# Performance work log

Hardware: AMD Instinct MI355X
Metric: run time of the kernel (lower is better)

The kernel has to match this reference:

```python
import jax, jax.numpy as jnp
import numpy as np

NUM_GRAPHS = 8
EV_A3_TO_GPA = 160.21766208


def _energy(pos, bond_vec, src, dst, edge_graph, centers, W1, b1, W2, b2, W3, b3):
    # Surrogate GNN energy: edge displacement mixes pos and bond_vec so both get grads,
    # mirroring grad(total_energies, [pos, bond_vec]) in the original wrapper.
    disp = bond_vec + pos[dst] - pos[src]                      # [E,3]
    d = jnp.sqrt(jnp.sum(disp * disp, axis=-1) + 1e-12)        # [E]
    rbf = jnp.exp(-jnp.square(d[:, None] - centers[None, :]))  # [E,K]
    h = jax.nn.silu(rbf @ W1 + b1)                             # [E,H]
    h = jax.nn.silu(h @ W2 + b2)                               # [E,H]
    e_edge = (h @ W3 + b3)[:, 0]                               # [E]
    return jax.ops.segment_sum(e_edge, edge_graph, num_segments=NUM_GRAPHS)  # [B]


def setup_inputs() -> dict:
    key = jax.random.key(0)
    ks = jax.random.split(key, 8)
    N, E, K, H = 49152, 786432, 32, 64
    pos = jax.random.normal(ks[0], (N, 3), jnp.float32) * 3.0
    bond_vec = jax.random.normal(ks[1], (E, 3), jnp.float32)
    src = jax.random.randint(ks[2], (E,), 0, N, dtype=jnp.int32)
    dst = jax.random.randint(ks[3], (E,), 0, N, dtype=jnp.int32)
    edge_graph = jnp.repeat(jnp.arange(NUM_GRAPHS, dtype=jnp.int32), E // NUM_GRAPHS)
    volume = jax.random.uniform(ks[4], (N,), jnp.float32, 50.0, 150.0)
    centers = jnp.linspace(0.0, 5.0, K).astype(jnp.float32)
    W1 = jax.random.normal(ks[5], (K, H), jnp.float32) / np.float32(np.sqrt(K))
    b1 = jnp.zeros((H,), jnp.float32)
    W2 = jax.random.normal(ks[6], (H, H), jnp.float32) / np.float32(np.sqrt(H))
    b2 = jnp.zeros((H,), jnp.float32)
    W3 = jax.random.normal(ks[7], (H, 1), jnp.float32) / np.float32(np.sqrt(H))
    b3 = jnp.zeros((1,), jnp.float32)
    return {"pos": pos, "bond_vec": bond_vec, "src": src, "dst": dst,
            "edge_graph": edge_graph, "volume": volume, "centers": centers,
            "W1": W1, "b1": b1, "W2": W2, "b2": b2, "W3": W3, "b3": b3}


def reference(pos, bond_vec, src, dst, edge_graph, volume, centers, W1, b1, W2, b2, W3, b3):
    energies, vjp_fn = jax.vjp(
        lambda p, bv: _energy(p, bv, src, dst, edge_graph, centers, W1, b1, W2, b2, W3, b3),
        pos, bond_vec)
    # grad_outputs = ones_like(total_energies)
    gpos, gbv = vjp_fn(jnp.ones_like(energies))
    forces = -gpos                                             # [N,3]
    f_ij = -gbv                                                # [E,3]
    # Per-graph stress: bond_vec_g^T @ f_ij_g, vectorized as segment-summed outer products.
    outer = bond_vec[:, :, None] * f_ij[:, None, :]            # [E,3,3]
    S = jax.ops.segment_sum(outer, edge_graph, num_segments=NUM_GRAPHS)  # [B,3,3]
    nodes_per_graph = pos.shape[0] // NUM_GRAPHS
    vol0 = volume[jnp.arange(NUM_GRAPHS) * nodes_per_graph]    # volume at first node of each graph
    stresses = (-EV_A3_TO_GPA * S / vol0[:, None, None]).reshape(NUM_GRAPHS * 3, 3)
    hessian = jnp.zeros((1,), jnp.float32)                     # calc_hessian=False
    return energies, forces, stresses, hessian
```

## Files before the change

### kernel.cpp

```cpp
#include <hip/hip_runtime.h>
#include <math.h>

#define K_RBF 32
#define H_DIM 64
#define TBL 4096
#define D_MAX 16.0f
#define N_NODES 49152
#define N_EDGES 786432
#define N_GRAPHS 8
#define NODES_PER_GRAPH 6144
#define EV_A3_TO_GPA 160.21766208f
#define LOG2E 1.44269504088896f

#define OUT_FORCES 8
#define OUT_STRESS 147464
#define OUT_TAIL_N 81

#define CHUNK_NODES  192
#define CHUNK_FLOATS 576
#define N_CHUNKS     256

#define EDGE_BLOCKS   512
#define EDGE_THREADS  512
#define EDGES_PER_THREAD 3
#define EDGES_PER_BLOCK (EDGE_THREADS * EDGES_PER_THREAD)
#define EDGES_PER_GRAPH (N_EDGES / N_GRAPHS)
#define BLK_PER_GRAPH 64

#define SLOT_CAP   40

#define LANES_PER_RUN 16
#define RUNS_PER_PASS 64
#define SCT_PASSES    8

#define OFF_TAB 0u
#define OFF_CNT 32768u
#define OFF_REC (32768u + (unsigned)(N_CHUNKS * EDGE_BLOCKS * 4))
#define WS_NEED ((size_t)OFF_REC + (size_t)N_CHUNKS * EDGE_BLOCKS * SLOT_CAP * 16u)

__device__ __forceinline__ int chunk_of(int node) {
    return (int)((unsigned)((node >> 6) * 683) >> 11);
}

__device__ __forceinline__ float2 mlp_entry(
    int i, int lane, const float* __restrict__ centers,
    const float* __restrict__ W1, const float* __restrict__ b1,
    const float* __restrict__ W2s, const float* __restrict__ b2,
    const float* __restrict__ W3, const float* __restrict__ b3)
{
    float d  = (float)i * (D_MAX / (float)TBL);
    float z1 = b1[lane], u = 0.f;
#pragma unroll
    for (int k = 0; k < K_RBF; ++k) {
        float tc = d - centers[k];
        float e  = exp2f(-tc * tc * LOG2E);
        float w  = W1[k * H_DIM + lane];
        z1 = fmaf(e, w, z1);
        u  = fmaf(-2.f * tc * e, w, u);
    }
    float s1  = 1.f / (1.f + exp2f(-z1 * LOG2E));
    float h1  = z1 * s1;
    float ds1 = s1 * fmaf(z1, 1.f - s1, 1.f);

    float z2 = b2[lane];
#pragma unroll
    for (int h = 0; h < H_DIM; ++h)
        z2 = fmaf(__shfl(h1, h, 64), W2s[h * 65 + lane], z2);

    float s2  = 1.f / (1.f + exp2f(-z2 * LOG2E));
    float w3  = W3[lane];
    float Fp  = z2 * s2 * w3;
    float dz2 = w3 * s2 * fmaf(z2, 1.f - s2, 1.f);

    float dh1 = 0.f;
#pragma unroll
    for (int j = 0; j < H_DIM; ++j)
        dh1 = fmaf(__shfl(dz2, j, 64), W2s[lane * 65 + j], dh1);

    float Gp = dh1 * ds1 * u;
#pragma unroll
    for (int m = 32; m > 0; m >>= 1) {
        Fp += __shfl_xor(Fp, m, 64);
        Gp += __shfl_xor(Gp, m, 64);
    }
    return make_float2(Fp + b3[0], Gp);
}

__global__ __launch_bounds__(256) void build_table(
    const float* __restrict__ centers,
    const float* __restrict__ W1, const float* __restrict__ b1,
    const float* __restrict__ W2, const float* __restrict__ b2,
    const float* __restrict__ W3, const float* __restrict__ b3,
    float2* __restrict__ tab, float* __restrict__ out, int zero_out_tail)
{
    if (blockIdx.x == 0 && zero_out_tail) {
        int t = threadIdx.x;
        if (t < N_GRAPHS) out[t] = 0.f;
        else if (t < OUT_TAIL_N) out[3 * N_NODES + t] = 0.f;
    }

    __shared__ float W2s[H_DIM * 65];
    for (int idx = threadIdx.x; idx < H_DIM * H_DIM; idx += 256)
        W2s[(idx >> 6) * 65 + (idx & 63)] = W2[idx];
    __syncthreads();

    int lane = threadIdx.x & 63;
    int i    = blockIdx.x * 4 + (threadIdx.x >> 6);
    float2 fg = mlp_entry(i, lane, centers, W1, b1, W2s, b2, W3, b3);
    if (lane == 0) tab[i] = fg;
}

__global__ __launch_bounds__(EDGE_THREADS) void edge_compute(
    const float* __restrict__ pos, const float* __restrict__ bond,
    const int* __restrict__ src, const int* __restrict__ dst,
    const float* __restrict__ volume, const float2* __restrict__ tab,
    float4* __restrict__ recs, int* __restrict__ cnttab,
    float* __restrict__ out)
{
    __shared__ int   cnt[N_CHUNKS];
    __shared__ float red[8][10];

    const int t = threadIdx.x;
    const int b = blockIdx.x;
    if (t < N_CHUNKS) cnt[t] = 0;
    __syncthreads();

    const int g = b >> 6;
    const int base_e = b * EDGES_PER_BLOCK;

    float vacc[10];
#pragma unroll
    for (int q = 0; q < 10; ++q) vacc[q] = 0.f;

#pragma unroll
    for (int i = 0; i < EDGES_PER_THREAD; ++i) {
        int e  = base_e + i * EDGE_THREADS + t;
        int si = src[e], di = dst[e];
        float bx = bond[3 * e + 0], by = bond[3 * e + 1], bz = bond[3 * e + 2];
        float dx = bx + pos[3 * di + 0] - pos[3 * si + 0];
        float dy = by + pos[3 * di + 1] - pos[3 * si + 1];
        float dz = bz + pos[3 * di + 2] - pos[3 * si + 2];
        float d  = sqrtf(fmaf(dx, dx, fmaf(dy, dy, fmaf(dz, dz, 1e-12f))));

        float tt  = fminf(d * ((float)TBL / D_MAX), (float)(TBL - 1));
        int   ix  = min((int)tt, TBL - 2);
        float fr  = tt - (float)ix;
        float2 ta = tab[ix], tb2 = tab[ix + 1];
        float F = fmaf(fr, tb2.x - ta.x, ta.x);
        float G = fmaf(fr, tb2.y - ta.y, ta.y);

        float scl = G / d;
        float gx = scl * dx, gy = scl * dy, gz = scl * dz;

        int c0 = chunk_of(di), c1 = chunk_of(si);
        int r0 = atomicAdd(&cnt[c0], 1);
        int r1 = atomicAdd(&cnt[c1], 1);
        if (r0 < SLOT_CAP)
            recs[((size_t)c0 * EDGE_BLOCKS + b) * SLOT_CAP + r0] =
                make_float4(-gx, -gy, -gz, __int_as_float(di - c0 * CHUNK_NODES));
        if (r1 < SLOT_CAP)
            recs[((size_t)c1 * EDGE_BLOCKS + b) * SLOT_CAP + r1] =
                make_float4(gx, gy, gz, __int_as_float(si - c1 * CHUNK_NODES));

        vacc[0] += F;
        vacc[1] = fmaf(bx, gx, vacc[1]); vacc[2] = fmaf(bx, gy, vacc[2]);
        vacc[3] = fmaf(bx, gz, vacc[3]); vacc[4] = fmaf(by, gx, vacc[4]);
        vacc[5] = fmaf(by, gy, vacc[5]); vacc[6] = fmaf(by, gz, vacc[6]);
        vacc[7] = fmaf(bz, gx, vacc[7]); vacc[8] = fmaf(bz, gy, vacc[8]);
        vacc[9] = fmaf(bz, gz, vacc[9]);
    }

#pragma unroll
    for (int q = 0; q < 10; ++q) {
        float x = vacc[q];
#pragma unroll
        for (int m = 32; m > 0; m >>= 1) x += __shfl_xor(x, m, 64);
        vacc[q] = x;
    }
    int wave = t >> 6;
    if ((t & 63) == 0)
#pragma unroll
        for (int q = 0; q < 10; ++q) red[wave][q] = vacc[q];
    __syncthreads();

    if (t < N_CHUNKS)
        cnttab[(size_t)t * EDGE_BLOCKS + b] = min(cnt[t], SLOT_CAP);

    if (t < 10) {
        float tot = 0.f;
#pragma unroll
        for (int k = 0; k < 8; ++k) tot += red[k][t];
        if (t == 0) atomicAdd(out + g, tot);
        else {
            float vol = volume[g * NODES_PER_GRAPH];
            atomicAdd(out + OUT_STRESS + g * 9 + (t - 1),
                      tot * (EV_A3_TO_GPA / vol));
        }
    }
}

__global__ __launch_bounds__(1024) void scatter_direct(
    const float4* __restrict__ recs, const int* __restrict__ cnttab,
    float* __restrict__ out)
{
    __shared__ float acc[CHUNK_FLOATS];
    __shared__ int   cl[EDGE_BLOCKS];
    const int t = threadIdx.x;
    const int c = blockIdx.x;
    if (t < CHUNK_FLOATS) acc[t] = 0.f;
    if (t < EDGE_BLOCKS) cl[t] = cnttab[(size_t)c * EDGE_BLOCKS + t];
    __syncthreads();

    const float4* seg = recs + (size_t)c * EDGE_BLOCKS * SLOT_CAP;
    const int sub = t & (LANES_PER_RUN - 1);
    const int rr0 = t >> 4;
#pragma unroll
    for (int p = 0; p < SCT_PASSES; ++p) {
        int rr  = p * RUNS_PER_PASS + rr0;
        int n   = cl[rr];
        const float4* run = seg + (size_t)rr * SLOT_CAP;
        for (int s = sub; s < n; s += LANES_PER_RUN) {
            float4 rec = run[s];
            int li = 3 * __float_as_int(rec.w);
            atomicAdd(&acc[li + 0], rec.x);
            atomicAdd(&acc[li + 1], rec.y);
            atomicAdd(&acc[li + 2], rec.z);
        }
    }
    __syncthreads();

    if (t < CHUNK_FLOATS)
        out[OUT_FORCES + c * CHUNK_FLOATS + t] = acc[t];
}

__global__ __launch_bounds__(256) void edge_fallback(
    const float* __restrict__ pos, const float* __restrict__ bond,
    const int* __restrict__ src, const int* __restrict__ dst,
    const float* __restrict__ volume, const float2* __restrict__ tab,
    float* __restrict__ out)
{
    __shared__ float red[4][10];
    int lb = (blockIdx.x & 7) * (EDGES_PER_GRAPH / 256) + (blockIdx.x >> 3);
    int g  = blockIdx.x & 7;
    int e  = lb * 256 + threadIdx.x;

    int si = src[e], di = dst[e];
    float bx = bond[3 * e + 0], by = bond[3 * e + 1], bz = bond[3 * e + 2];
    float dx = bx + pos[3 * di + 0] - pos[3 * si + 0];
    float dy = by + pos[3 * di + 1] - pos[3 * si + 1];
    float dz = bz + pos[3 * di + 2] - pos[3 * si + 2];
    float d  = sqrtf(fmaf(dx, dx, fmaf(dy, dy, fmaf(dz, dz, 1e-12f))));

    float tt  = fminf(d * ((float)TBL / D_MAX), (float)(TBL - 1));
    int   ix  = min((int)tt, TBL - 2);
    float fr  = tt - (float)ix;
    float2 ta = tab[ix], tb2 = tab[ix + 1];
    float F = fmaf(fr, tb2.x - ta.x, ta.x);
    float G = fmaf(fr, tb2.y - ta.y, ta.y);
    float scl = G / d;
    float gx = scl * dx, gy = scl * dy, gz = scl * dz;

    float* forces = out + OUT_FORCES;
    atomicAdd(forces + 3 * di + 0, -gx);
    atomicAdd(forces + 3 * di + 1, -gy);
    atomicAdd(forces + 3 * di + 2, -gz);
    atomicAdd(forces + 3 * si + 0,  gx);
    atomicAdd(forces + 3 * si + 1,  gy);
    atomicAdd(forces + 3 * si + 2,  gz);

    float v[10] = { F,
                    bx * gx, bx * gy, bx * gz,
                    by * gx, by * gy, by * gz,
                    bz * gx, bz * gy, bz * gz };
#pragma unroll
    for (int q = 0; q < 10; ++q) {
        float x = v[q];
#pragma unroll
        for (int m = 32; m > 0; m >>= 1) x += __shfl_xor(x, m, 64);
        v[q] = x;
    }
    int wave = threadIdx.x >> 6;
    if ((threadIdx.x & 63) == 0)
#pragma unroll
        for (int q = 0; q < 10; ++q) red[wave][q] = v[q];
    __syncthreads();
    if (threadIdx.x < 10) {
        float tot = red[0][threadIdx.x] + red[1][threadIdx.x]
                  + red[2][threadIdx.x] + red[3][threadIdx.x];
        if (threadIdx.x == 0) atomicAdd(out + g, tot);
        else {
            float vol = volume[g * NODES_PER_GRAPH];
            atomicAdd(out + OUT_STRESS + g * 9 + (threadIdx.x - 1),
                      tot * (EV_A3_TO_GPA / vol));
        }
    }
}

extern "C" void kernel_launch(void* const* d_in, const int* in_sizes, int n_in,
                              void* d_out, int out_size, void* d_ws, size_t ws_size,
                              hipStream_t stream)
{
    const float* pos     = (const float*)d_in[0];
    const float* bond    = (const float*)d_in[1];
    const int*   src     = (const int*)d_in[2];
    const int*   dst     = (const int*)d_in[3];
    const float* volume  = (const float*)d_in[5];
    const float* centers = (const float*)d_in[6];
    const float* W1 = (const float*)d_in[7];
    const float* b1 = (const float*)d_in[8];
    const float* W2 = (const float*)d_in[9];
    const float* b2 = (const float*)d_in[10];
    const float* W3 = (const float*)d_in[11];
    const float* b3 = (const float*)d_in[12];
    float*  out    = (float*)d_out;
    char*   ws     = (char*)d_ws;
    float2* tab    = (float2*)(ws + OFF_TAB);
    int*    cnttab = (int*)(ws + OFF_CNT);
    float4* recs   = (float4*)(ws + OFF_REC);

    if (ws_size >= WS_NEED) {
        build_table<<<TBL / 4, 256, 0, stream>>>(centers, W1, b1, W2, b2, W3, b3,
                                                 tab, out, 1);
        edge_compute<<<EDGE_BLOCKS, EDGE_THREADS, 0, stream>>>(
            pos, bond, src, dst, volume, tab, recs, cnttab, out);
        scatter_direct<<<N_CHUNKS, 1024, 0, stream>>>(recs, cnttab, out);
    } else {
        hipMemsetAsync(d_out, 0, (size_t)out_size * sizeof(float), stream);
        build_table<<<TBL / 4, 256, 0, stream>>>(centers, W1, b1, W2, b2, W3, b3,
                                                 tab, out, 0);
        edge_fallback<<<N_EDGES / 256, 256, 0, stream>>>(
            pos, bond, src, dst, volume, tab, out);
    }
}
```

Before: 154.4 us.

## Replace bucketed record scatter with direct global atomic force accumulation

Removes the two-pass scheme, in which per-chunk force records went to workspace and a separate scatter kernel reduced them in shared memory. Edge threads now atomically add force contributions straight into global memory after a memset, and the edge kernel is relaunched with more, smaller blocks. This saves the record write/read traffic and one kernel launch. In exchange it adds 6 global float atomics per edge with random addresses and a memset of the whole output.

Measured after the change: 346.5 us. 2.24x slower.

```diff
diff --git a/kernel.cpp b/kernel.cpp
--- a/kernel.cpp
+++ b/kernel.cpp
@@ -14,33 +14,16 @@
 
 #define OUT_FORCES 8
 #define OUT_STRESS 147464
-#define OUT_TAIL_N 81
 
-#define CHUNK_NODES  192
-#define CHUNK_FLOATS 576
-#define N_CHUNKS     256
-
-#define EDGE_BLOCKS   512
-#define EDGE_THREADS  512
+#define EDGE_BLOCKS   1024
+#define EDGE_THREADS  256
 #define EDGES_PER_THREAD 3
 #define EDGES_PER_BLOCK (EDGE_THREADS * EDGES_PER_THREAD)
 #define EDGES_PER_GRAPH (N_EDGES / N_GRAPHS)
-#define BLK_PER_GRAPH 64
-
-#define SLOT_CAP   40
-
-#define LANES_PER_RUN 16
-#define RUNS_PER_PASS 64
-#define SCT_PASSES    8
+#define BLK_PER_GRAPH 128
 
 #define OFF_TAB 0u
-#define OFF_CNT 32768u
-#define OFF_REC (32768u + (unsigned)(N_CHUNKS * EDGE_BLOCKS * 4))
-#define WS_NEED ((size_t)OFF_REC + (size_t)N_CHUNKS * EDGE_BLOCKS * SLOT_CAP * 16u)
-
-__device__ __forceinline__ int chunk_of(int node) {
-    return (int)((unsigned)((node >> 6) * 683) >> 11);
-}
+#define WS_NEED 32768u
 
 __device__ __forceinline__ float2 mlp_entry(
     int i, int lane, const float* __restrict__ centers,
@@ -91,14 +74,8 @@
     const float* __restrict__ W1, const float* __restrict__ b1,
     const float* __restrict__ W2, const float* __restrict__ b2,
     const float* __restrict__ W3, const float* __restrict__ b3,
-    float2* __restrict__ tab, float* __restrict__ out, int zero_out_tail)
+    float2* __restrict__ tab)
 {
-    if (blockIdx.x == 0 && zero_out_tail) {
-        int t = threadIdx.x;
-        if (t < N_GRAPHS) out[t] = 0.f;
-        else if (t < OUT_TAIL_N) out[3 * N_NODES + t] = 0.f;
-    }
-
     __shared__ float W2s[H_DIM * 65];
     for (int idx = threadIdx.x; idx < H_DIM * H_DIM; idx += 256)
         W2s[(idx >> 6) * 65 + (idx & 63)] = W2[idx];
@@ -110,23 +87,19 @@
     if (lane == 0) tab[i] = fg;
 }
 
-__global__ __launch_bounds__(EDGE_THREADS) void edge_compute(
+__global__ __launch_bounds__(EDGE_THREADS) void edge_direct(
     const float* __restrict__ pos, const float* __restrict__ bond,
     const int* __restrict__ src, const int* __restrict__ dst,
     const float* __restrict__ volume, const float2* __restrict__ tab,
-    float4* __restrict__ recs, int* __restrict__ cnttab,
     float* __restrict__ out)
 {
-    __shared__ int   cnt[N_CHUNKS];
-    __shared__ float red[8][10];
+    __shared__ float red[4][10];
 
     const int t = threadIdx.x;
     const int b = blockIdx.x;
-    if (t < N_CHUNKS) cnt[t] = 0;
-    __syncthreads();
-
-    const int g = b >> 6;
+    const int g = b >> 7;
     const int base_e = b * EDGES_PER_BLOCK;
+    float* __restrict__ forces = out + OUT_FORCES;
 
     float vacc[10];
 #pragma unroll
@@ -152,15 +125,12 @@
         float scl = G / d;
         float gx = scl * dx, gy = scl * dy, gz = scl * dz;
 
-        int c0 = chunk_of(di), c1 = chunk_of(si);
-        int r0 = atomicAdd(&cnt[c0], 1);
-        int r1 = atomicAdd(&cnt[c1], 1);
-        if (r0 < SLOT_CAP)
-            recs[((size_t)c0 * EDGE_BLOCKS + b) * SLOT_CAP + r0] =
-                make_float4(-gx, -gy, -gz, __int_as_float(di - c0 * CHUNK_NODES));
-        if (r1 < SLOT_CAP)
-            recs[((size_t)c1 * EDGE_BLOCKS + b) * SLOT_CAP + r1] =
-                make_float4(gx, gy, gz, __int_as_float(si - c1 * CHUNK_NODES));
+        atomicAdd(forces + 3 * di + 0, -gx);
+        atomicAdd(forces + 3 * di + 1, -gy);
+        atomicAdd(forces + 3 * di + 2, -gz);
+        atomicAdd(forces + 3 * si + 0,  gx);
+        atomicAdd(forces + 3 * si + 1,  gy);
+        atomicAdd(forces + 3 * si + 2,  gz);
 
         vacc[0] += F;
         vacc[1] = fmaf(bx, gx, vacc[1]); vacc[2] = fmaf(bx, gy, vacc[2]);
@@ -182,115 +152,12 @@
 #pragma unroll
         for (int q = 0; q < 10; ++q) red[wave][q] = vacc[q];
     __syncthreads();
-
-    if (t < N_CHUNKS)
-        cnttab[(size_t)t * EDGE_BLOCKS + b] = min(cnt[t], SLOT_CAP);
-
     if (t < 10) {
-        float tot = 0.f;
-#pragma unroll
-        for (int k = 0; k < 8; ++k) tot += red[k][t];
+        float tot = red[0][t] + red[1][t] + red[2][t] + red[3][t];
         if (t == 0) atomicAdd(out + g, tot);
         else {
             float vol = volume[g * NODES_PER_GRAPH];
             atomicAdd(out + OUT_STRESS + g * 9 + (t - 1),
-                      tot * (EV_A3_TO_GPA / vol));
-        }
-    }
-}
-
-__global__ __launch_bounds__(1024) void scatter_direct(
-    const float4* __restrict__ recs, const int* __restrict__ cnttab,
-    float* __restrict__ out)
-{
-    __shared__ float acc[CHUNK_FLOATS];
-    __shared__ int   cl[EDGE_BLOCKS];
-    const int t = threadIdx.x;
-    const int c = blockIdx.x;
-    if (t < CHUNK_FLOATS) acc[t] = 0.f;
-    if (t < EDGE_BLOCKS) cl[t] = cnttab[(size_t)c * EDGE_BLOCKS + t];
-    __syncthreads();
-
-    const float4* seg = recs + (size_t)c * EDGE_BLOCKS * SLOT_CAP;
-    const int sub = t & (LANES_PER_RUN - 1);
-    const int rr0 = t >> 4;
-#pragma unroll
-    for (int p = 0; p < SCT_PASSES; ++p) {
-        int rr  = p * RUNS_PER_PASS + rr0;
-        int n   = cl[rr];
-        const float4* run = seg + (size_t)rr * SLOT_CAP;
-        for (int s = sub; s < n; s += LANES_PER_RUN) {
-            float4 rec = run[s];
-            int li = 3 * __float_as_int(rec.w);
-            atomicAdd(&acc[li + 0], rec.x);
-            atomicAdd(&acc[li + 1], rec.y);
-            atomicAdd(&acc[li + 2], rec.z);
-        }
-    }
-    __syncthreads();
-
-    if (t < CHUNK_FLOATS)
-        out[OUT_FORCES + c * CHUNK_FLOATS + t] = acc[t];
-}
-
-__global__ __launch_bounds__(256) void edge_fallback(
-    const float* __restrict__ pos, const float* __restrict__ bond,
-    const int* __restrict__ src, const int* __restrict__ dst,
-    const float* __restrict__ volume, const float2* __restrict__ tab,
-    float* __restrict__ out)
-{
-    __shared__ float red[4][10];
-    int lb = (blockIdx.x & 7) * (EDGES_PER_GRAPH / 256) + (blockIdx.x >> 3);
-    int g  = blockIdx.x & 7;
-    int e  = lb * 256 + threadIdx.x;
-
-    int si = src[e], di = dst[e];
-    float bx = bond[3 * e + 0], by = bond[3 * e + 1], bz = bond[3 * e + 2];
-    float dx = bx + pos[3 * di + 0] - pos[3 * si + 0];
-    float dy = by + pos[3 * di + 1] - pos[3 * si + 1];
-    float dz = bz + pos[3 * di + 2] - pos[3 * si + 2];
-    float d  = sqrtf(fmaf(dx, dx, fmaf(dy, dy, fmaf(dz, dz, 1e-12f))));
-
-    float tt  = fminf(d * ((float)TBL / D_MAX), (float)(TBL - 1));
-    int   ix  = min((int)tt, TBL - 2);
-    float fr  = tt - (float)ix;
-    float2 ta = tab[ix], tb2 = tab[ix + 1];
-    float F = fmaf(fr, tb2.x - ta.x, ta.x);
-    float G = fmaf(fr, tb2.y - ta.y, ta.y);
-    float scl = G / d;
-    float gx = scl * dx, gy = scl * dy, gz = scl * dz;
-
-    float* forces = out + OUT_FORCES;
-    atomicAdd(forces + 3 * di + 0, -gx);
-    atomicAdd(forces + 3 * di + 1, -gy);
-    atomicAdd(forces + 3 * di + 2, -gz);
-    atomicAdd(forces + 3 * si + 0,  gx);
-    atomicAdd(forces + 3 * si + 1,  gy);
-    atomicAdd(forces + 3 * si + 2,  gz);
-
-    float v[10] = { F,
-                    bx * gx, bx * gy, bx * gz,
-                    by * gx, by * gy, by * gz,
-                    bz * gx, bz * gy, bz * gz };
-#pragma unroll
-    for (int q = 0; q < 10; ++q) {
-        float x = v[q];
-#pragma unroll
-        for (int m = 32; m > 0; m >>= 1) x += __shfl_xor(x, m, 64);
-        v[q] = x;
-    }
-    int wave = threadIdx.x >> 6;
-    if ((threadIdx.x & 63) == 0)
-#pragma unroll
-        for (int q = 0; q < 10; ++q) red[wave][q] = v[q];
-    __syncthreads();
-    if (threadIdx.x < 10) {
-        float tot = red[0][threadIdx.x] + red[1][threadIdx.x]
-                  + red[2][threadIdx.x] + red[3][threadIdx.x];
-        if (threadIdx.x == 0) atomicAdd(out + g, tot);
-        else {
-            float vol = volume[g * NODES_PER_GRAPH];
-            atomicAdd(out + OUT_STRESS + g * 9 + (threadIdx.x - 1),
                       tot * (EV_A3_TO_GPA / vol));
         }
     }
@@ -312,23 +179,13 @@
     const float* b2 = (const float*)d_in[10];
     const float* W3 = (const float*)d_in[11];
     const float* b3 = (const float*)d_in[12];
-    float*  out    = (float*)d_out;
-    char*   ws     = (char*)d_ws;
-    float2* tab    = (float2*)(ws + OFF_TAB);
-    int*    cnttab = (int*)(ws + OFF_CNT);
-    float4* recs   = (float4*)(ws + OFF_REC);
+    float*  out = (float*)d_out;
+    char*   ws  = (char*)d_ws;
+    float2* tab = (float2*)(ws + OFF_TAB);
 
-    if (ws_size >= WS_NEED) {
-        build_table<<<TBL / 4, 256, 0, stream>>>(centers, W1, b1, W2, b2, W3, b3,
-                                                 tab, out, 1);
-        edge_compute<<<EDGE_BLOCKS, EDGE_THREADS, 0, stream>>>(
-            pos, bond, src, dst, volume, tab, recs, cnttab, out);
-        scatter_direct<<<N_CHUNKS, 1024, 0, stream>>>(recs, cnttab, out);
-    } else {
-        hipMemsetAsync(d_out, 0, (size_t)out_size * sizeof(float), stream);
-        build_table<<<TBL / 4, 256, 0, stream>>>(centers, W1, b1, W2, b2, W3, b3,
-                                                 tab, out, 0);
-        edge_fallback<<<N_EDGES / 256, 256, 0, stream>>>(
-            pos, bond, src, dst, volume, tab, out);
-    }
+    hipMemsetAsync(d_out, 0, (size_t)out_size * sizeof(float), stream);
+    build_table<<<TBL / 4, 256, 0, stream>>>(centers, W1, b1, W2, b2, W3, b3, tab);
+    edge_direct<<<EDGE_BLOCKS, EDGE_THREADS, 0, stream>>>(
+        pos, bond, src, dst, volume, tab, out);
+    (void)ws_size; (void)in_sizes; (void)n_in;
 }
```
